# Optimization experiments

Hardware: AMD Instinct MI355X
Metric: run time of the kernel (lower is better)

Reference implementation:

```python
import jax, jax.numpy as jnp
import numpy as np

N_GRAM = 3
N_HEAD = 8


def setup_inputs() -> dict:
    key = jax.random.key(0)
    ks = jax.random.split(key, 8)
    V, E, H, H2, C, B, L = 50000, 512, 512, 512, 10, 64, 512
    def rn(k, shape, scale):
        return jax.random.normal(k, shape, jnp.float32) * jnp.float32(scale)
    return {
        "x": jax.random.randint(ks[0], (B, L), 0, V),
        "emb": rn(ks[1], (V, E), 0.02),
        "Wq": rn(ks[2], (H, E), 1.0 / np.sqrt(H)),
        "Wx": rn(ks[3], (E, 3 * H), 1.0 / np.sqrt(E)),
        "Wh": rn(ks[4], (H, 3 * H), 1.0 / np.sqrt(H)),
        "bx": jnp.zeros((3 * H,), jnp.float32),
        "bh": jnp.zeros((3 * H,), jnp.float32),
        "W1": rn(ks[5], (H, H2), 1.0 / np.sqrt(H)),
        "b1": jnp.zeros((H2,), jnp.float32),
        "W2": rn(ks[6], (H2, C), 1.0 / np.sqrt(H2)),
        "b2": jnp.zeros((C,), jnp.float32),
    }


def _gru_ngram_attn(xe, Wq, Wx, Wh, bx, bh):
    # xe: [B, L, E] embedded sequence
    B, L, E = xe.shape
    g, nh = N_GRAM, N_HEAD
    hd = E // nh
    H = Wh.shape[0]
    scale = jnp.float32(1.0 / np.sqrt(hd))
    xpad = jnp.pad(xe, ((0, 0), (g - 1, 0), (0, 0)))
    win = jnp.stack([xpad[:, i:i + L] for i in range(g)], axis=2)  # [B,L,g,E]
    win_t = jnp.transpose(win, (1, 0, 2, 3))  # [L,B,g,E] for scan
    h0 = jnp.zeros((B, H), xe.dtype)

    def step(h, w):
        # multi-head dot attention: query from prev hidden, keys/values = n-gram window
        q = (h @ Wq).reshape(B, nh, hd)          # [B,nh,hd]
        k = w.reshape(B, g, nh, hd)              # [B,g,nh,hd]
        scores = jnp.einsum('bnd,bgnd->bng', q, k) * scale
        a = jax.nn.softmax(scores, axis=-1)      # over window positions
        ctx = jnp.einsum('bng,bgnd->bnd', a, k).reshape(B, E)
        # GRU cell with attended context as input
        gx = ctx @ Wx + bx
        gh = h @ Wh + bh
        xr, xz, xn = jnp.split(gx, 3, axis=-1)
        hr, hz, hn = jnp.split(gh, 3, axis=-1)
        r = jax.nn.sigmoid(xr + hr)
        z = jax.nn.sigmoid(xz + hz)
        n = jnp.tanh(xn + r * hn)
        hnew = (1.0 - z) * n + z * h
        return hnew, hnew

    _, hs = jax.lax.scan(step, h0, win_t)  # [L,B,H]
    return hs


def reference(x, emb, Wq, Wx, Wh, bx, bh, W1, b1, W2, b2):
    xe = emb[x]  # [B,L,E]
    hs = _gru_ngram_attn(xe, Wq, Wx, Wh, bx, bh)  # [L,B,H]
    pooled = jax.nn.relu(hs.sum(axis=0))          # sum over seq, then relu
    out = pooled @ W1 + b1                        # fc1 path (H != embed not needed; H is GRU out)
    out = out @ W2 + b2                           # [B,C]
    return out
```

## Files before the change

kernel.cpp:

```cpp
#include <hip/hip_runtime.h>
#include <hip/hip_fp16.h>

typedef __attribute__((ext_vector_type(2))) _Float16 half2v;
typedef __attribute__((ext_vector_type(2))) __fp16   fp16x2;

#define SEQ     512
#define THREADS 512

#define WQ_OFF   0
#define WX_OFF   32768
#define WH_OFF   131072
#define SYNC_OFF 3670016

__device__ inline unsigned int pack2f16(float a, float b) {
    fp16x2 p = __builtin_amdgcn_cvt_pkrtz(a, b);
    return __builtin_bit_cast(unsigned int, p);
}
__device__ inline float fdot2u(unsigned int a, unsigned int b, float acc) {
    return __builtin_amdgcn_fdot2(__builtin_bit_cast(half2v, a),
                                  __builtin_bit_cast(half2v, b), acc, false);
}
__device__ inline float dot4(uint4 h, uint4 w, float acc) {
    acc = fdot2u(h.x, w.x, acc); acc = fdot2u(h.y, w.y, acc);
    acc = fdot2u(h.z, w.z, acc); acc = fdot2u(h.w, w.w, acc);
    return acc;
}
__device__ inline float fsigmoid(float x) { return 1.f / (1.f + __expf(-x)); }
__device__ inline float ftanhf(float x) {
    float e = __expf(-2.f * fabsf(x));
    float t = (1.f - e) / (1.f + e);
    return copysignf(t, x);
}
__device__ inline void vmem_fence() { asm volatile("s_waitcnt vmcnt(0)" ::: "memory"); }
__device__ inline unsigned a_ld(unsigned* p) {
    return __hip_atomic_load(p, __ATOMIC_RELAXED, __HIP_MEMORY_SCOPE_AGENT);
}
__device__ inline void a_st(unsigned* p, unsigned v) {
    __hip_atomic_store(p, v, __ATOMIC_RELAXED, __HIP_MEMORY_SCOPE_AGENT);
}
__device__ inline float a_ldf(float* p) {
    return __hip_atomic_load(p, __ATOMIC_RELAXED, __HIP_MEMORY_SCOPE_AGENT);
}
__device__ inline void a_stf(float* p, float v) {
    __hip_atomic_store(p, v, __ATOMIC_RELAXED, __HIP_MEMORY_SCOPE_AGENT);
}

__global__ __launch_bounds__(256)
void pack_weights(const float* __restrict__ Wq,
                  const float* __restrict__ Wx,
                  const float* __restrict__ Wh,
                  uint4* __restrict__ ws) {
    int tid = blockIdx.x * blockDim.x + threadIdx.x;
    const float* src; uint4* dst; int C, idx;
    if (tid < 64 * 512)                  { src = Wq; dst = ws;          C = 512;  idx = tid; }
    else if (tid < 64 * 512 + 64 * 1536) { src = Wx; dst = ws + WX_OFF; C = 1536; idx = tid - 64 * 512; }
    else                                 { src = Wh; dst = ws + WH_OFF; C = 1536; idx = tid - (64 * 512 + 64 * 1536); }
    int m4 = idx / C;
    int c  = idx - m4 * C;
    const float* s = src + (size_t)(m4 * 8) * C + c;
    uint4 o;
    o.x = pack2f16(s[0 * (size_t)C], s[1 * (size_t)C]);
    o.y = pack2f16(s[2 * (size_t)C], s[3 * (size_t)C]);
    o.z = pack2f16(s[4 * (size_t)C], s[5 * (size_t)C]);
    o.w = pack2f16(s[6 * (size_t)C], s[7 * (size_t)C]);
    dst[idx] = o;
}

__global__ __launch_bounds__(THREADS)
void gru_scan(const int* __restrict__ xtok, const float* __restrict__ emb,
              const uint4* __restrict__ wsp, const float* __restrict__ bx,
              const float* __restrict__ bh, const float* __restrict__ W1,
              const float* __restrict__ b1, const float* __restrict__ W2,
              const float* __restrict__ b2, float* __restrict__ out)
{
    const int blk  = blockIdx.x;
    const int gid  = blk & 7;
    const int bid  = blk >> 3;
    const int tid  = threadIdx.x;
    const int lane = tid & 63;
    const int wid  = tid >> 6;
    const int colsub = lane & 7;
    const int bp     = (lane >> 3) & 3;
    const int chsub  = lane >> 5;

    char* syncb = (char*)wsp + SYNC_OFF;
    unsigned* flagH = (unsigned*)syncb;
    unsigned* flagS = (unsigned*)(syncb + 1024);
    unsigned* Hbuf  = (unsigned*)(syncb + 2048);
    float* Pbuf     = (float*)(syncb + 133120);
    float* pooled_g = (float*)(syncb + 182272);
    float* fc1_g    = (float*)(syncb + 313344);

    __shared__ uint4 lds_W [64][65];
    __shared__ uint4 lds_Wx[64][49];
    __shared__ uint4 lds_h4[8][65];
    __shared__ unsigned u_pk[3][8][48][4];
    __shared__ float redQf[1152];
    __shared__ float redH[8][48][9];
    __shared__ float a_all[8][8][3];

    for (int i = tid; i < 64 * 64; i += THREADS) {
        int ch = i >> 6, cl = i & 63;
        uint4 v;
        if (cl < 16) v = wsp[WQ_OFF + ch * 512 + bid * 16 + cl];
        else { int g = (cl - 16) >> 4, c = (cl - 16) & 15;
               v = wsp[WH_OFF + ch * 1536 + g * 512 + bid * 16 + c]; }
        lds_W[ch][cl] = v;
    }
    for (int i = tid; i < 64 * 48; i += THREADS) {
        int ch = i / 48, cl = i - ch * 48;
        int g = cl >> 4, c = cl & 15;
        lds_Wx[ch][cl] = wsp[WX_OFF + ch * 1536 + g * 512 + bid * 16 + c];
    }

    float bxr = 0, bxz = 0, bxn = 0, bhr = 0, bhz = 0, bhn = 0;
    if (tid < 128) {
        int c = tid >> 3, cg = bid * 16 + c;
        bxr = bx[cg]; bxz = bx[512 + cg]; bxn = bx[1024 + cg];
        bhr = bh[cg]; bhz = bh[512 + cg]; bhn = bh[1024 + cg];
    }

    const int gb = gid * 8 + wid;
    {
        int tk = xtok[gb * SEQ];
        const float4* p = (const float4*)(emb + (size_t)tk * 512 + lane * 8);
        float4 ra = p[0], rb = p[1];
        uint4 pk;
        pk.x = pack2f16(ra.x, ra.y); pk.y = pack2f16(ra.z, ra.w);
        pk.z = pack2f16(rb.x, rb.y); pk.w = pack2f16(rb.z, rb.w);
        lds_h4[wid][lane] = pk;
        unsigned* up = &u_pk[0][0][0][0];
        for (int i = tid; i < 3072; i += THREADS) up[1536 + i] = 0u;
    }
    float hprev = 0.f, pooledv = 0.f;
    __syncthreads();

    for (int t = 0; t < SEQ; ++t) {
        const int par = t & 1;
        const int slot = t % 3;

        int tnext = (t + 1 < SEQ) ? (t + 1) : t;
        int tkn = xtok[gb * SEQ + tnext];
        const float4* pn = (const float4*)(emb + (size_t)tkn * 512 + lane * 8);
        float4 r3a = pn[0], r3b = pn[1];

        float winv[16];
        int b3 = 0, g3 = 0, trow = -1;
        if (wid == 0 && lane < 24) {
            b3 = lane / 3; g3 = lane - b3 * 3;
            trow = t - 2 + g3;
            int tok = (trow >= 0) ? xtok[(gid * 8 + b3) * SEQ + trow] : -1;
            if (tok >= 0) {
                const float* er = emb + (size_t)tok * 512 + bid * 16;
                #pragma unroll
                for (int d = 0; d < 16; ++d) winv[d] = er[d];
            } else {
                #pragma unroll
                for (int d = 0; d < 16; ++d) winv[d] = 0.f;
            }
        }

        {
            float acu[12];
            #pragma unroll
            for (int i = 0; i < 12; ++i) acu[i] = 0.f;
            int ch0 = wid * 8 + chsub * 4;
            #pragma unroll
            for (int i = 0; i < 4; ++i) {
                int ch = ch0 + i;
                uint4 c0 = lds_h4[bp][ch], c1 = lds_h4[bp + 4][ch];
                #pragma unroll
                for (int j = 0; j < 6; ++j) {
                    uint4 w = lds_Wx[ch][colsub + 8 * j];
                    acu[j]     = dot4(c0, w, acu[j]);
                    acu[6 + j] = dot4(c1, w, acu[6 + j]);
                }
            }
            #pragma unroll
            for (int i = 0; i < 12; ++i) acu[i] += __shfl_xor(acu[i], 32);
            if (chsub == 0) {
                #pragma unroll
                for (int j = 0; j < 6; ++j)
                    u_pk[slot][wid][colsub + 8 * j][bp] = pack2f16(acu[j], acu[6 + j]);
            }
        }

        if (wid == 0) {
            bool done = lane >= 32;
            while (!__all(done)) {
                if (!done) done = (a_ld(&flagH[gid * 32 + lane]) >= (unsigned)t);
                if (!__all(done)) __builtin_amdgcn_s_sleep(1);
            }
        }
        __syncthreads();

        {
            int bb = tid >> 6, c4 = tid & 63;
            unsigned* s = Hbuf + (size_t)(par ^ 1) * 16384 + (gid * 8 + bb) * 256 + c4 * 4;
            uint4 v;
            v.x = a_ld(s); v.y = a_ld(s + 1); v.z = a_ld(s + 2); v.w = a_ld(s + 3);
            lds_h4[bb][c4] = v;
        }
        __syncthreads();

        {
            float aq0 = 0, aq1 = 0, aq2 = 0, aq3 = 0;
            int ch0 = wid * 8 + chsub * 4;
            #pragma unroll
            for (int i = 0; i < 4; ++i) {
                int ch = ch0 + i;
                uint4 h0 = lds_h4[bp][ch], h1 = lds_h4[bp + 4][ch];
                uint4 w0 = lds_W[ch][colsub], w1 = lds_W[ch][colsub + 8];
                aq0 = dot4(h0, w0, aq0); aq1 = dot4(h0, w1, aq1);
                aq2 = dot4(h1, w0, aq2); aq3 = dot4(h1, w1, aq3);
            }
            aq0 += __shfl_xor(aq0, 32); aq1 += __shfl_xor(aq1, 32);
            aq2 += __shfl_xor(aq2, 32); aq3 += __shfl_xor(aq3, 32);
            if (chsub == 0) {
                redQf[(wid * 16 + colsub) * 9 + bp]         = aq0;
                redQf[(wid * 16 + colsub + 8) * 9 + bp]     = aq1;
                redQf[(wid * 16 + colsub) * 9 + bp + 4]     = aq2;
                redQf[(wid * 16 + colsub + 8) * 9 + bp + 4] = aq3;
            }
        }
        __syncthreads();

        if (wid == 0) {
            if (lane < 24) {
                float s = 0.f;
                if (trow >= 0) {
                    #pragma unroll
                    for (int d = 0; d < 16; ++d) {
                        float q = redQf[d * 9 + b3];
                        #pragma unroll
                        for (int k = 1; k < 8; ++k) q += redQf[(k * 16 + d) * 9 + b3];
                        s += winv[d] * q;
                    }
                }
                a_stf(&Pbuf[(size_t)((par * 8 + gid) * 32 + bid) * 24 + b3 * 3 + g3], s);
            }
            vmem_fence();
            if (lane == 0) a_st(&flagS[gid * 32 + bid], (unsigned)(t + 1));
            bool done = lane >= 32;
            while (!__all(done)) {
                if (!done) done = (a_ld(&flagS[gid * 32 + lane]) >= (unsigned)(t + 1));
                if (!__all(done)) __builtin_amdgcn_s_sleep(1);
            }
            {
                int bb = lane >> 3, n = lane & 7;
                float* pb = Pbuf + (size_t)(par * 8 + gid) * 32 * 24;
                float sc0 = 0, sc1 = 0, sc2 = 0;
                #pragma unroll
                for (int j = 0; j < 4; ++j) {
                    float* pj = pb + (n * 4 + j) * 24 + bb * 3;
                    sc0 += a_ldf(pj); sc1 += a_ldf(pj + 1); sc2 += a_ldf(pj + 2);
                }
                sc0 *= 0.125f; sc1 *= 0.125f; sc2 *= 0.125f;
                float mx = fmaxf(sc0, fmaxf(sc1, sc2));
                float e0 = __expf(sc0 - mx), e1 = __expf(sc1 - mx), e2 = __expf(sc2 - mx);
                float inv = 1.f / (e0 + e1 + e2);
                a_all[bb][n][0] = e0 * inv; a_all[bb][n][1] = e1 * inv; a_all[bb][n][2] = e2 * inv;
            }
        } else {
            #pragma unroll 1
            for (int rep = 0; rep < 2; ++rep) {
                int k = (rep == 0) ? wid : 0;
                if (rep == 1 && wid != 7) break;
                float ag[12];
                #pragma unroll
                for (int i = 0; i < 12; ++i) ag[i] = 0.f;
                int ch0 = k * 8 + chsub * 4;
                #pragma unroll
                for (int i = 0; i < 4; ++i) {
                    int ch = ch0 + i;
                    uint4 h0 = lds_h4[bp][ch], h1 = lds_h4[bp + 4][ch];
                    #pragma unroll
                    for (int j = 0; j < 6; ++j) {
                        uint4 w = lds_W[ch][16 + colsub + 8 * j];
                        ag[j]     = dot4(h0, w, ag[j]);
                        ag[6 + j] = dot4(h1, w, ag[6 + j]);
                    }
                }
                #pragma unroll
                for (int i = 0; i < 12; ++i) ag[i] += __shfl_xor(ag[i], 32);
                if (chsub == 0) {
                    #pragma unroll
                    for (int j = 0; j < 6; ++j) {
                        redH[k][colsub + 8 * j][bp]     = ag[j];
                        redH[k][colsub + 8 * j][bp + 4] = ag[6 + j];
                    }
                }
            }
        }
        __syncthreads();

        if (tid >= 64 && tid < 448) {
            int idx = tid - 64;
            int col = idx >> 3, bb = idx & 7;
            float ghs = redH[0][col][bb];
            #pragma unroll
            for (int k = 1; k < 8; ++k) ghs += redH[k][col][bb];
            float gxs = 0.f;
            int half = bb >> 2, bq = bb & 3;
            #pragma unroll
            for (int g = 0; g < 3; ++g) {
                int sg = (t + 1 + g) % 3;
                #pragma unroll
                for (int k = 0; k < 8; ++k) {
                    fp16x2 uv = __builtin_bit_cast(fp16x2, u_pk[sg][k][col][bq]);
                    gxs += a_all[bb][k][g] * (float)uv[half];
                }
            }
            redQf[col * 8 + bb]       = ghs;
            redQf[384 + col * 8 + bb] = gxs;
        }
        {
            uint4 pk;
            pk.x = pack2f16(r3a.x, r3a.y); pk.y = pack2f16(r3a.z, r3a.w);
            pk.z = pack2f16(r3b.x, r3b.y); pk.w = pack2f16(r3b.z, r3b.w);
            lds_h4[wid][lane] = pk;
        }
        __syncthreads();

        if (tid < 128) {
            int c = tid >> 3, bb = tid & 7;
            float ghr = redQf[c * 8 + bb]        + bhr;
            float ghz = redQf[(16 + c) * 8 + bb] + bhz;
            float ghn = redQf[(32 + c) * 8 + bb] + bhn;
            float gxr = redQf[384 + c * 8 + bb]        + bxr;
            float gxz = redQf[384 + (16 + c) * 8 + bb] + bxz;
            float gxn = redQf[384 + (32 + c) * 8 + bb] + bxn;
            float r = fsigmoid(gxr + ghr);
            float z = fsigmoid(gxz + ghz);
            float n = ftanhf(gxn + r * ghn);
            float hnew = (1.f - z) * n + z * hprev;
            hprev = hnew; pooledv += hnew;
            float hnext = __shfl_down(hnew, 8);
            if ((c & 1) == 0)
                a_st(&Hbuf[(size_t)par * 16384 + (gid * 8 + bb) * 256 + bid * 8 + (c >> 1)],
                     pack2f16(hnew, hnext));
        }
        vmem_fence();
        __syncthreads();
        if (tid == 0) a_st(&flagH[gid * 32 + bid], (unsigned)(t + 1));
    }

    float* stage = (float*)&lds_W[0][0];
    if (tid < 128) {
        int c = tid >> 3, bb = tid & 7;
        a_stf(&pooled_g[(gid * 8 + bb) * 512 + bid * 16 + c], fmaxf(pooledv, 0.f));
    }
    vmem_fence();
    __syncthreads();
    if (tid == 0) a_st(&flagS[gid * 32 + bid], (unsigned)(SEQ + 1));
    if (wid == 0) {
        bool done = lane >= 32;
        while (!__all(done)) {
            if (!done) done = (a_ld(&flagS[gid * 32 + lane]) >= (unsigned)(SEQ + 1));
            if (!__all(done)) __builtin_amdgcn_s_sleep(1);
        }
    }
    __syncthreads();

    for (int i = tid; i < 8 * 512; i += THREADS) {
        int bb = i >> 9, k = i & 511;
        stage[bb * 512 + k] = a_ldf(&pooled_g[(gid * 8 + bb) * 512 + k]);
    }
    __syncthreads();

    if (tid < 128) {
        int c = tid >> 3, bb = tid & 7;
        int cg = bid * 16 + c;
        const float* pr = stage + bb * 512;
        float acc1 = b1[cg];
        for (int k = 0; k < 512; ++k) acc1 += pr[k] * W1[(size_t)k * 512 + cg];
        a_stf(&fc1_g[(gid * 8 + bb) * 512 + cg], acc1);
    }
    vmem_fence();
    __syncthreads();
    if (tid == 0) a_st(&flagH[gid * 32 + bid], (unsigned)(SEQ + 2));

    if (bid == 0) {
        if (wid == 0) {
            bool done = lane >= 32;
            while (!__all(done)) {
                if (!done) done = (a_ld(&flagH[gid * 32 + lane]) >= (unsigned)(SEQ + 2));
                if (!__all(done)) __builtin_amdgcn_s_sleep(1);
            }
        }
        __syncthreads();
        for (int i = tid; i < 8 * 512; i += THREADS) {
            int bb = i >> 9, k = i & 511;
            stage[bb * 512 + k] = a_ldf(&fc1_g[(gid * 8 + bb) * 512 + k]);
        }
        __syncthreads();
        if (tid < 80) {
            int bb = tid / 10, cls = tid - bb * 10;
            const float* fr = stage + bb * 512;
            float a2 = b2[cls];
            for (int k = 0; k < 512; ++k) a2 += fr[k] * W2[k * 10 + cls];
            out[(gid * 8 + bb) * 10 + cls] = a2;
        }
    }
}

extern "C" void kernel_launch(void* const* d_in, const int* in_sizes, int n_in,
                              void* d_out, int out_size, void* d_ws, size_t ws_size,
                              hipStream_t stream) {
    const int*   x   = (const int*)d_in[0];
    const float* emb = (const float*)d_in[1];
    const float* Wq  = (const float*)d_in[2];
    const float* Wx  = (const float*)d_in[3];
    const float* Wh  = (const float*)d_in[4];
    const float* bx  = (const float*)d_in[5];
    const float* bh  = (const float*)d_in[6];
    const float* W1  = (const float*)d_in[7];
    const float* b1  = (const float*)d_in[8];
    const float* W2  = (const float*)d_in[9];
    const float* b2  = (const float*)d_in[10];
    uint4* wsp = (uint4*)d_ws;
    float* outp = (float*)d_out;

    hipLaunchKernelGGL(pack_weights, dim3(896), dim3(256), 0, stream, Wq, Wx, Wh, wsp);
    hipMemsetAsync((char*)d_ws + SYNC_OFF, 0, 182272, stream);

    void* args[] = { (void*)&x, (void*)&emb, (void*)&wsp, (void*)&bx, (void*)&bh,
                     (void*)&W1, (void*)&b1, (void*)&W2, (void*)&b2, (void*)&outp };
    hipError_t e = hipLaunchCooperativeKernel((void*)gru_scan, dim3(256), dim3(THREADS),
                                              args, 0, stream);
    if (e != hipSuccess) {
        hipLaunchKernelGGL(gru_scan, dim3(256), dim3(THREADS), 0, stream,
                           x, emb, wsp, bx, bh, W1, b1, W2, b2, outp);
    }
}
```

Baseline: 3.621 ms.

## Split each XCD's batch into two interleaved half-groups to overlap cross-block sync

```diff
diff --git a/kernel.cpp b/kernel.cpp
--- a/kernel.cpp
+++ b/kernel.cpp
@@ -74,30 +74,36 @@
               const float* __restrict__ b2, float* __restrict__ out)
 {
     const int blk  = blockIdx.x;
-    const int gid  = blk & 7;
+    const int xcd  = blk & 7;
     const int bid  = blk >> 3;
+    const int gA   = xcd * 2;
+    const int gB   = xcd * 2 + 1;
     const int tid  = threadIdx.x;
     const int lane = tid & 63;
-    const int wid  = tid >> 6;
+    const int w    = tid >> 6;
     const int colsub = lane & 7;
     const int bp     = (lane >> 3) & 3;
     const int chsub  = lane >> 5;
 
     char* syncb = (char*)wsp + SYNC_OFF;
     unsigned* flagH = (unsigned*)syncb;
-    unsigned* flagS = (unsigned*)(syncb + 1024);
-    unsigned* Hbuf  = (unsigned*)(syncb + 2048);
-    float* Pbuf     = (float*)(syncb + 133120);
-    float* pooled_g = (float*)(syncb + 182272);
-    float* fc1_g    = (float*)(syncb + 313344);
-
-    __shared__ uint4 lds_W [64][65];
-    __shared__ uint4 lds_Wx[64][49];
-    __shared__ uint4 lds_h4[8][65];
-    __shared__ unsigned u_pk[3][8][48][4];
-    __shared__ float redQf[1152];
-    __shared__ float redH[8][48][9];
-    __shared__ float a_all[8][8][3];
+    unsigned* flagS = (unsigned*)(syncb + 2048);
+    unsigned* Hbuf  = (unsigned*)(syncb + 4096);
+    float* Pbuf     = (float*)(syncb + 135168);
+    float* pooled_g = (float*)(syncb + 184320);
+    float* fc1_g    = (float*)(syncb + 315392);
+    unsigned* flagP = (unsigned*)(syncb + 446464);
+    unsigned* flagF = (unsigned*)(syncb + 447488);
+
+    __shared__ uint4 lds_W  [64][64];
+    __shared__ uint4 lds_Wx [64][48];
+    __shared__ uint4 lds_win[2][4][65];
+    __shared__ uint4 lds_hb [4][65];
+    __shared__ unsigned u_pk  [2][3][8][48][2];
+    __shared__ unsigned redH_pk[2][8][48][2];
+    __shared__ float redQf[640];
+    __shared__ float ghs[240], gxs[240];
+    __shared__ float a_all[2][4][8][3];
 
     for (int i = tid; i < 64 * 64; i += THREADS) {
         int ch = i >> 6, cl = i & 63;
@@ -115,283 +121,440 @@
 
     float bxr = 0, bxz = 0, bxn = 0, bhr = 0, bhz = 0, bhn = 0;
     if (tid < 128) {
-        int c = tid >> 3, cg = bid * 16 + c;
+        int m = (tid & 63) >> 2, cg = bid * 16 + m;
         bxr = bx[cg]; bxz = bx[512 + cg]; bxn = bx[1024 + cg];
         bhr = bh[cg]; bhz = bh[512 + cg]; bhn = bh[1024 + cg];
     }
 
-    const int gb = gid * 8 + wid;
+    const int wg  = w >> 2;
+    const int wb  = w & 3;
+    const int gbw = (xcd * 2 + wg) * 4 + wb;
+
     {
-        int tk = xtok[gb * SEQ];
+        int tk = xtok[gbw * SEQ];
         const float4* p = (const float4*)(emb + (size_t)tk * 512 + lane * 8);
         float4 ra = p[0], rb = p[1];
         uint4 pk;
         pk.x = pack2f16(ra.x, ra.y); pk.y = pack2f16(ra.z, ra.w);
         pk.z = pack2f16(rb.x, rb.y); pk.w = pack2f16(rb.z, rb.w);
-        lds_h4[wid][lane] = pk;
-        unsigned* up = &u_pk[0][0][0][0];
-        for (int i = tid; i < 3072; i += THREADS) up[1536 + i] = 0u;
+        lds_win[wg][wb][lane] = pk;
+        unsigned* up = &u_pk[0][0][0][0][0];
+        for (int i = tid; i < 2 * 1536; i += THREADS) {
+            int G = i / 1536, off = i - G * 1536;
+            up[G * 2304 + 768 + off] = 0u;
+        }
     }
     float hprev = 0.f, pooledv = 0.f;
     __syncthreads();
 
     for (int t = 0; t < SEQ; ++t) {
-        const int par = t & 1;
+        const int par  = t & 1;
         const int slot = t % 3;
 
-        int tnext = (t + 1 < SEQ) ? (t + 1) : t;
-        int tkn = xtok[gb * SEQ + tnext];
+        int tnext = (t + 1 < SEQ) ? t + 1 : t;
+        int tkn = xtok[gbw * SEQ + tnext];
         const float4* pn = (const float4*)(emb + (size_t)tkn * 512 + lane * 8);
         float4 r3a = pn[0], r3b = pn[1];
 
         float winv[16];
-        int b3 = 0, g3 = 0, trow = -1;
-        if (wid == 0 && lane < 24) {
-            b3 = lane / 3; g3 = lane - b3 * 3;
-            trow = t - 2 + g3;
-            int tok = (trow >= 0) ? xtok[(gid * 8 + b3) * SEQ + trow] : -1;
-            if (tok >= 0) {
-                const float* er = emb + (size_t)tok * 512 + bid * 16;
-                #pragma unroll
-                for (int d = 0; d < 16; ++d) winv[d] = er[d];
-            } else {
-                #pragma unroll
-                for (int d = 0; d < 16; ++d) winv[d] = 0.f;
-            }
-        }
-
-        {
-            float acu[12];
-            #pragma unroll
-            for (int i = 0; i < 12; ++i) acu[i] = 0.f;
-            int ch0 = wid * 8 + chsub * 4;
-            #pragma unroll
-            for (int i = 0; i < 4; ++i) {
-                int ch = ch0 + i;
-                uint4 c0 = lds_h4[bp][ch], c1 = lds_h4[bp + 4][ch];
-                #pragma unroll
-                for (int j = 0; j < 6; ++j) {
-                    uint4 w = lds_Wx[ch][colsub + 8 * j];
-                    acu[j]     = dot4(c0, w, acu[j]);
-                    acu[6 + j] = dot4(c1, w, acu[6 + j]);
-                }
-            }
-            #pragma unroll
-            for (int i = 0; i < 12; ++i) acu[i] += __shfl_xor(acu[i], 32);
-            if (chsub == 0) {
-                #pragma unroll
-                for (int j = 0; j < 6; ++j)
-                    u_pk[slot][wid][colsub + 8 * j][bp] = pack2f16(acu[j], acu[6 + j]);
-            }
-        }
-
-        if (wid == 0) {
+        int b3 = 0, g3 = 0, trow = -1, sgrp = -1;
+        if (w == 0) {
+            int l = -1;
+            if (lane < 12)                     { sgrp = 0; l = lane; }
+            else if (lane >= 32 && lane < 44)  { sgrp = 1; l = lane - 32; }
+            if (sgrp >= 0) {
+                b3 = l / 3; g3 = l - b3 * 3; trow = t - 2 + g3;
+                int gg = xcd * 2 + sgrp;
+                int tok = (trow >= 0) ? xtok[(gg * 4 + b3) * SEQ + trow] : -1;
+                if (tok >= 0) {
+                    const float* er = emb + (size_t)tok * 512 + bid * 16;
+                    #pragma unroll
+                    for (int d = 0; d < 16; ++d) winv[d] = er[d];
+                } else {
+                    #pragma unroll
+                    for (int d = 0; d < 16; ++d) winv[d] = 0.f;
+                }
+            }
+        }
+
+        uint4 hregA, hregB;
+
+        if (w == 0) {
             bool done = lane >= 32;
             while (!__all(done)) {
-                if (!done) done = (a_ld(&flagH[gid * 32 + lane]) >= (unsigned)t);
+                if (!done) done = (a_ld(&flagH[gA * 32 + lane]) >= (unsigned)t);
                 if (!__all(done)) __builtin_amdgcn_s_sleep(1);
-            }
-        }
-        __syncthreads();
-
-        {
-            int bb = tid >> 6, c4 = tid & 63;
-            unsigned* s = Hbuf + (size_t)(par ^ 1) * 16384 + (gid * 8 + bb) * 256 + c4 * 4;
-            uint4 v;
-            v.x = a_ld(s); v.y = a_ld(s + 1); v.z = a_ld(s + 2); v.w = a_ld(s + 3);
-            lds_h4[bb][c4] = v;
-        }
-        __syncthreads();
-
-        {
-            float aq0 = 0, aq1 = 0, aq2 = 0, aq3 = 0;
-            int ch0 = wid * 8 + chsub * 4;
-            #pragma unroll
-            for (int i = 0; i < 4; ++i) {
-                int ch = ch0 + i;
-                uint4 h0 = lds_h4[bp][ch], h1 = lds_h4[bp + 4][ch];
-                uint4 w0 = lds_W[ch][colsub], w1 = lds_W[ch][colsub + 8];
-                aq0 = dot4(h0, w0, aq0); aq1 = dot4(h0, w1, aq1);
-                aq2 = dot4(h1, w0, aq2); aq3 = dot4(h1, w1, aq3);
-            }
-            aq0 += __shfl_xor(aq0, 32); aq1 += __shfl_xor(aq1, 32);
-            aq2 += __shfl_xor(aq2, 32); aq3 += __shfl_xor(aq3, 32);
-            if (chsub == 0) {
-                redQf[(wid * 16 + colsub) * 9 + bp]         = aq0;
-                redQf[(wid * 16 + colsub + 8) * 9 + bp]     = aq1;
-                redQf[(wid * 16 + colsub) * 9 + bp + 4]     = aq2;
-                redQf[(wid * 16 + colsub + 8) * 9 + bp + 4] = aq3;
-            }
-        }
-        __syncthreads();
-
-        if (wid == 0) {
-            if (lane < 24) {
-                float s = 0.f;
-                if (trow >= 0) {
-                    #pragma unroll
-                    for (int d = 0; d < 16; ++d) {
-                        float q = redQf[d * 9 + b3];
-                        #pragma unroll
-                        for (int k = 1; k < 8; ++k) q += redQf[(k * 16 + d) * 9 + b3];
-                        s += winv[d] * q;
-                    }
-                }
-                a_stf(&Pbuf[(size_t)((par * 8 + gid) * 32 + bid) * 24 + b3 * 3 + g3], s);
-            }
-            vmem_fence();
-            if (lane == 0) a_st(&flagS[gid * 32 + bid], (unsigned)(t + 1));
-            bool done = lane >= 32;
-            while (!__all(done)) {
-                if (!done) done = (a_ld(&flagS[gid * 32 + lane]) >= (unsigned)(t + 1));
-                if (!__all(done)) __builtin_amdgcn_s_sleep(1);
-            }
-            {
-                int bb = lane >> 3, n = lane & 7;
-                float* pb = Pbuf + (size_t)(par * 8 + gid) * 32 * 24;
-                float sc0 = 0, sc1 = 0, sc2 = 0;
-                #pragma unroll
-                for (int j = 0; j < 4; ++j) {
-                    float* pj = pb + (n * 4 + j) * 24 + bb * 3;
-                    sc0 += a_ldf(pj); sc1 += a_ldf(pj + 1); sc2 += a_ldf(pj + 2);
-                }
-                sc0 *= 0.125f; sc1 *= 0.125f; sc2 *= 0.125f;
-                float mx = fmaxf(sc0, fmaxf(sc1, sc2));
-                float e0 = __expf(sc0 - mx), e1 = __expf(sc1 - mx), e2 = __expf(sc2 - mx);
-                float inv = 1.f / (e0 + e1 + e2);
-                a_all[bb][n][0] = e0 * inv; a_all[bb][n][1] = e1 * inv; a_all[bb][n][2] = e2 * inv;
             }
         } else {
             #pragma unroll 1
             for (int rep = 0; rep < 2; ++rep) {
-                int k = (rep == 0) ? wid : 0;
-                if (rep == 1 && wid != 7) break;
-                float ag[12];
-                #pragma unroll
-                for (int i = 0; i < 12; ++i) ag[i] = 0.f;
+                int k = (rep == 0) ? w : 0;
+                if (rep == 1 && w != 7) break;
+                float acu[6];
+                #pragma unroll
+                for (int i = 0; i < 6; ++i) acu[i] = 0.f;
                 int ch0 = k * 8 + chsub * 4;
                 #pragma unroll
                 for (int i = 0; i < 4; ++i) {
-                    int ch = ch0 + i;
-                    uint4 h0 = lds_h4[bp][ch], h1 = lds_h4[bp + 4][ch];
-                    #pragma unroll
-                    for (int j = 0; j < 6; ++j) {
-                        uint4 w = lds_W[ch][16 + colsub + 8 * j];
-                        ag[j]     = dot4(h0, w, ag[j]);
-                        ag[6 + j] = dot4(h1, w, ag[6 + j]);
+                    uint4 c0 = lds_win[0][bp][ch0 + i];
+                    #pragma unroll
+                    for (int j = 0; j < 6; ++j)
+                        acu[j] = dot4(c0, lds_Wx[ch0 + i][colsub + 8 * j], acu[j]);
+                }
+                #pragma unroll
+                for (int j = 0; j < 6; ++j) {
+                    acu[j] += __shfl_xor(acu[j], 32);
+                    float hi = __shfl_down(acu[j], 16);
+                    if (chsub == 0 && bp < 2)
+                        u_pk[0][slot][k][colsub + 8 * j][bp] = pack2f16(acu[j], hi);
+                }
+            }
+        }
+        __syncthreads();
+        if (tid < 256) {
+            int bb = tid >> 6, ch = tid & 63;
+            unsigned* s = Hbuf + (size_t)(par ^ 1) * 16384 + (gA * 4 + bb) * 256 + ch * 4;
+            hregA.x = a_ld(s); hregA.y = a_ld(s + 1); hregA.z = a_ld(s + 2); hregA.w = a_ld(s + 3);
+        }
+
+        if (w == 0) {
+            bool done = lane >= 32;
+            while (!__all(done)) {
+                if (!done) done = (a_ld(&flagH[gB * 32 + lane]) >= (unsigned)t);
+                if (!__all(done)) __builtin_amdgcn_s_sleep(1);
+            }
+        } else {
+            #pragma unroll 1
+            for (int rep = 0; rep < 2; ++rep) {
+                int k = (rep == 0) ? w : 0;
+                if (rep == 1 && w != 7) break;
+                float acu[6];
+                #pragma unroll
+                for (int i = 0; i < 6; ++i) acu[i] = 0.f;
+                int ch0 = k * 8 + chsub * 4;
+                #pragma unroll
+                for (int i = 0; i < 4; ++i) {
+                    uint4 c0 = lds_win[1][bp][ch0 + i];
+                    #pragma unroll
+                    for (int j = 0; j < 6; ++j)
+                        acu[j] = dot4(c0, lds_Wx[ch0 + i][colsub + 8 * j], acu[j]);
+                }
+                #pragma unroll
+                for (int j = 0; j < 6; ++j) {
+                    acu[j] += __shfl_xor(acu[j], 32);
+                    float hi = __shfl_down(acu[j], 16);
+                    if (chsub == 0 && bp < 2)
+                        u_pk[1][slot][k][colsub + 8 * j][bp] = pack2f16(acu[j], hi);
+                }
+            }
+        }
+        __syncthreads();
+        if (tid < 256) {
+            int bb = tid >> 6, ch = tid & 63;
+            unsigned* s = Hbuf + (size_t)(par ^ 1) * 16384 + (gB * 4 + bb) * 256 + ch * 4;
+            hregB.x = a_ld(s); hregB.y = a_ld(s + 1); hregB.z = a_ld(s + 2); hregB.w = a_ld(s + 3);
+        }
+
+        if (tid < 256) lds_hb[tid >> 6][tid & 63] = hregA;
+        __syncthreads();
+        {
+            float aq0 = 0, aq1 = 0;
+            int ch0 = w * 8 + chsub * 4;
+            #pragma unroll
+            for (int i = 0; i < 4; ++i) {
+                uint4 h0 = lds_hb[bp][ch0 + i];
+                aq0 = dot4(h0, lds_W[ch0 + i][colsub],     aq0);
+                aq1 = dot4(h0, lds_W[ch0 + i][colsub + 8], aq1);
+            }
+            aq0 += __shfl_xor(aq0, 32); aq1 += __shfl_xor(aq1, 32);
+            if (chsub == 0) {
+                redQf[w * 80 + colsub * 5 + bp]       = aq0;
+                redQf[w * 80 + (colsub + 8) * 5 + bp] = aq1;
+            }
+        }
+        __syncthreads();
+        if (w == 0) {
+            if (sgrp == 0) {
+                float s = 0.f;
+                if (trow >= 0) {
+                    #pragma unroll
+                    for (int d = 0; d < 16; ++d) {
+                        float q = redQf[d * 5 + b3];
+                        #pragma unroll
+                        for (int k = 1; k < 8; ++k) q += redQf[k * 80 + d * 5 + b3];
+                        s += winv[d] * q;
                     }
                 }
-                #pragma unroll
-                for (int i = 0; i < 12; ++i) ag[i] += __shfl_xor(ag[i], 32);
-                if (chsub == 0) {
-                    #pragma unroll
-                    for (int j = 0; j < 6; ++j) {
-                        redH[k][colsub + 8 * j][bp]     = ag[j];
-                        redH[k][colsub + 8 * j][bp + 4] = ag[6 + j];
+                a_stf(&Pbuf[((size_t)(par * 16 + gA) * 32 + bid) * 12 + b3 * 3 + g3], s);
+            }
+            vmem_fence();
+            if (lane == 0) a_st(&flagS[gA * 32 + bid], (unsigned)(t + 1));
+        } else {
+            #pragma unroll 1
+            for (int rep = 0; rep < 2; ++rep) {
+                int k = (rep == 0) ? w : 0;
+                if (rep == 1 && w != 7) break;
+                float ag[6];
+                #pragma unroll
+                for (int i = 0; i < 6; ++i) ag[i] = 0.f;
+                int ch0 = k * 8 + chsub * 4;
+                #pragma unroll
+                for (int i = 0; i < 4; ++i) {
+                    uint4 h0 = lds_hb[bp][ch0 + i];
+                    #pragma unroll
+                    for (int j = 0; j < 6; ++j)
+                        ag[j] = dot4(h0, lds_W[ch0 + i][16 + colsub + 8 * j], ag[j]);
+                }
+                #pragma unroll
+                for (int j = 0; j < 6; ++j) {
+                    ag[j] += __shfl_xor(ag[j], 32);
+                    float hi = __shfl_down(ag[j], 16);
+                    if (chsub == 0 && bp < 2)
+                        redH_pk[0][k][colsub + 8 * j][bp] = pack2f16(ag[j], hi);
+                }
+            }
+        }
+
+        __syncthreads();
+        if (tid < 256) lds_hb[tid >> 6][tid & 63] = hregB;
+        __syncthreads();
+        {
+            float aq0 = 0, aq1 = 0;
+            int ch0 = w * 8 + chsub * 4;
+            #pragma unroll
+            for (int i = 0; i < 4; ++i) {
+                uint4 h0 = lds_hb[bp][ch0 + i];
+                aq0 = dot4(h0, lds_W[ch0 + i][colsub],     aq0);
+                aq1 = dot4(h0, lds_W[ch0 + i][colsub + 8], aq1);
+            }
+            aq0 += __shfl_xor(aq0, 32); aq1 += __shfl_xor(aq1, 32);
+            if (chsub == 0) {
+                redQf[w * 80 + colsub * 5 + bp]       = aq0;
+                redQf[w * 80 + (colsub + 8) * 5 + bp] = aq1;
+            }
+        }
+        __syncthreads();
+        if (w == 0) {
+            if (sgrp == 1) {
+                float s = 0.f;
+                if (trow >= 0) {
+                    #pragma unroll
+                    for (int d = 0; d < 16; ++d) {
+                        float q = redQf[d * 5 + b3];
+                        #pragma unroll
+                        for (int k = 1; k < 8; ++k) q += redQf[k * 80 + d * 5 + b3];
+                        s += winv[d] * q;
                     }
                 }
-            }
-        }
-        __syncthreads();
-
-        if (tid >= 64 && tid < 448) {
-            int idx = tid - 64;
-            int col = idx >> 3, bb = idx & 7;
-            float ghs = redH[0][col][bb];
-            #pragma unroll
-            for (int k = 1; k < 8; ++k) ghs += redH[k][col][bb];
-            float gxs = 0.f;
-            int half = bb >> 2, bq = bb & 3;
-            #pragma unroll
-            for (int g = 0; g < 3; ++g) {
-                int sg = (t + 1 + g) % 3;
-                #pragma unroll
-                for (int k = 0; k < 8; ++k) {
-                    fp16x2 uv = __builtin_bit_cast(fp16x2, u_pk[sg][k][col][bq]);
-                    gxs += a_all[bb][k][g] * (float)uv[half];
-                }
-            }
-            redQf[col * 8 + bb]       = ghs;
-            redQf[384 + col * 8 + bb] = gxs;
+                a_stf(&Pbuf[((size_t)(par * 16 + gB) * 32 + bid) * 12 + b3 * 3 + g3], s);
+            }
+            vmem_fence();
+            if (lane == 0) a_st(&flagS[gB * 32 + bid], (unsigned)(t + 1));
+        } else {
+            #pragma unroll 1
+            for (int rep = 0; rep < 2; ++rep) {
+                int k = (rep == 0) ? w : 0;
+                if (rep == 1 && w != 7) break;
+                float ag[6];
+                #pragma unroll
+                for (int i = 0; i < 6; ++i) ag[i] = 0.f;
+                int ch0 = k * 8 + chsub * 4;
+                #pragma unroll
+                for (int i = 0; i < 4; ++i) {
+                    uint4 h0 = lds_hb[bp][ch0 + i];
+                    #pragma unroll
+                    for (int j = 0; j < 6; ++j)
+                        ag[j] = dot4(h0, lds_W[ch0 + i][16 + colsub + 8 * j], ag[j]);
+                }
+                #pragma unroll
+                for (int j = 0; j < 6; ++j) {
+                    ag[j] += __shfl_xor(ag[j], 32);
+                    float hi = __shfl_down(ag[j], 16);
+                    if (chsub == 0 && bp < 2)
+                        redH_pk[1][k][colsub + 8 * j][bp] = pack2f16(ag[j], hi);
+                }
+            }
+        }
+
+        if (w == 0) {
+            bool done = lane >= 32;
+            while (!__all(done)) {
+                if (!done) done = (a_ld(&flagS[gA * 32 + lane]) >= (unsigned)(t + 1));
+                if (!__all(done)) __builtin_amdgcn_s_sleep(1);
+            }
+            if (lane < 32) {
+                int b = lane >> 3, n = lane & 7;
+                float* base = Pbuf + (size_t)(par * 16 + gA) * 32 * 12;
+                float s0 = 0, s1 = 0, s2 = 0;
+                #pragma unroll
+                for (int j = 0; j < 4; ++j) {
+                    float* pj = base + (n * 4 + j) * 12 + b * 3;
+                    s0 += a_ldf(pj); s1 += a_ldf(pj + 1); s2 += a_ldf(pj + 2);
+                }
+                s0 *= 0.125f; s1 *= 0.125f; s2 *= 0.125f;
+                float mx = fmaxf(s0, fmaxf(s1, s2));
+                float e0 = __expf(s0 - mx), e1 = __expf(s1 - mx), e2 = __expf(s2 - mx);
+                float inv = 1.f / (e0 + e1 + e2);
+                a_all[0][b][n][0] = e0 * inv; a_all[0][b][n][1] = e1 * inv; a_all[0][b][n][2] = e2 * inv;
+            }
         }
         {
             uint4 pk;
             pk.x = pack2f16(r3a.x, r3a.y); pk.y = pack2f16(r3a.z, r3a.w);
             pk.z = pack2f16(r3b.x, r3b.y); pk.w = pack2f16(r3b.z, r3b.w);
-            lds_h4[wid][lane] = pk;
-        }
-        __syncthreads();
-
-        if (tid < 128) {
-            int c = tid >> 3, bb = tid & 7;
-            float ghr = redQf[c * 8 + bb]        + bhr;
-            float ghz = redQf[(16 + c) * 8 + bb] + bhz;
-            float ghn = redQf[(32 + c) * 8 + bb] + bhn;
-            float gxr = redQf[384 + c * 8 + bb]        + bxr;
-            float gxz = redQf[384 + (16 + c) * 8 + bb] + bxz;
-            float gxn = redQf[384 + (32 + c) * 8 + bb] + bxn;
-            float r = fsigmoid(gxr + ghr);
-            float z = fsigmoid(gxz + ghz);
-            float n = ftanhf(gxn + r * ghn);
+            lds_win[wg][wb][lane] = pk;
+        }
+        __syncthreads();
+        if (tid < 192) {
+            int col = tid >> 2, b = tid & 3;
+            int bq = b & 1, hf = b >> 1;
+            float ghsum = 0.f;
+            #pragma unroll
+            for (int k = 0; k < 8; ++k) {
+                fp16x2 v = __builtin_bit_cast(fp16x2, redH_pk[0][k][col][bq]);
+                ghsum += (float)v[hf];
+            }
+            float gxsum = 0.f;
+            #pragma unroll
+            for (int g = 0; g < 3; ++g) {
+                int sg = (t + 1 + g) % 3;
+                #pragma unroll
+                for (int k = 0; k < 8; ++k) {
+                    fp16x2 u = __builtin_bit_cast(fp16x2, u_pk[0][sg][k][col][bq]);
+                    gxsum += a_all[0][b][k][g] * (float)u[hf];
+                }
+            }
+            ghs[col * 5 + b] = ghsum;
+            gxs[col * 5 + b] = gxsum;
+        }
+        __syncthreads();
+        if (tid < 64) {
+            int m = tid >> 2, b = tid & 3;
+            float r = fsigmoid(gxs[m * 5 + b] + bxr + ghs[m * 5 + b] + bhr);
+            float z = fsigmoid(gxs[(16 + m) * 5 + b] + bxz + ghs[(16 + m) * 5 + b] + bhz);
+            float n = ftanhf(gxs[(32 + m) * 5 + b] + bxn + r * (ghs[(32 + m) * 5 + b] + bhn));
             float hnew = (1.f - z) * n + z * hprev;
             hprev = hnew; pooledv += hnew;
-            float hnext = __shfl_down(hnew, 8);
-            if ((c & 1) == 0)
-                a_st(&Hbuf[(size_t)par * 16384 + (gid * 8 + bb) * 256 + bid * 8 + (c >> 1)],
-                     pack2f16(hnew, hnext));
+            float hnx = __shfl_down(hnew, 4);
+            if (!(m & 1))
+                a_st(&Hbuf[(size_t)par * 16384 + (gA * 4 + b) * 256 + bid * 8 + (m >> 1)],
+                     pack2f16(hnew, hnx));
         }
         vmem_fence();
         __syncthreads();
-        if (tid == 0) a_st(&flagH[gid * 32 + bid], (unsigned)(t + 1));
-    }
-
-    float* stage = (float*)&lds_W[0][0];
+        if (tid == 0) a_st(&flagH[gA * 32 + bid], (unsigned)(t + 1));
+
+        if (w == 0) {
+            bool done = lane >= 32;
+            while (!__all(done)) {
+                if (!done) done = (a_ld(&flagS[gB * 32 + lane]) >= (unsigned)(t + 1));
+                if (!__all(done)) __builtin_amdgcn_s_sleep(1);
+            }
+            if (lane < 32) {
+                int b = lane >> 3, n = lane & 7;
+                float* base = Pbuf + (size_t)(par * 16 + gB) * 32 * 12;
+                float s0 = 0, s1 = 0, s2 = 0;
+                #pragma unroll
+                for (int j = 0; j < 4; ++j) {
+                    float* pj = base + (n * 4 + j) * 12 + b * 3;
+                    s0 += a_ldf(pj); s1 += a_ldf(pj + 1); s2 += a_ldf(pj + 2);
+                }
+                s0 *= 0.125f; s1 *= 0.125f; s2 *= 0.125f;
+                float mx = fmaxf(s0, fmaxf(s1, s2));
+                float e0 = __expf(s0 - mx), e1 = __expf(s1 - mx), e2 = __expf(s2 - mx);
+                float inv = 1.f / (e0 + e1 + e2);
+                a_all[1][b][n][0] = e0 * inv; a_all[1][b][n][1] = e1 * inv; a_all[1][b][n][2] = e2 * inv;
+            }
+        }
+        __syncthreads();
+        if (tid < 192) {
+            int col = tid >> 2, b = tid & 3;
+            int bq = b & 1, hf = b >> 1;
+            float ghsum = 0.f;
+            #pragma unroll
+            for (int k = 0; k < 8; ++k) {
+                fp16x2 v = __builtin_bit_cast(fp16x2, redH_pk[1][k][col][bq]);
+                ghsum += (float)v[hf];
+            }
+            float gxsum = 0.f;
+            #pragma unroll
+            for (int g = 0; g < 3; ++g) {
+                int sg = (t + 1 + g) % 3;
+                #pragma unroll
+                for (int k = 0; k < 8; ++k) {
+                    fp16x2 u = __builtin_bit_cast(fp16x2, u_pk[1][sg][k][col][bq]);
+                    gxsum += a_all[1][b][k][g] * (float)u[hf];
+                }
+            }
+            ghs[col * 5 + b] = ghsum;
+            gxs[col * 5 + b] = gxsum;
+        }
+        __syncthreads();
+        if (tid >= 64 && tid < 128) {
+            int m = (tid & 63) >> 2, b = (tid & 63) & 3;
+            float r = fsigmoid(gxs[m * 5 + b] + bxr + ghs[m * 5 + b] + bhr);
+            float z = fsigmoid(gxs[(16 + m) * 5 + b] + bxz + ghs[(16 + m) * 5 + b] + bhz);
+            float n = ftanhf(gxs[(32 + m) * 5 + b] + bxn + r * (ghs[(32 + m) * 5 + b] + bhn));
+            float hnew = (1.f - z) * n + z * hprev;
+            hprev = hnew; pooledv += hnew;
+            float hnx = __shfl_down(hnew, 4);
+            if (!(m & 1))
+                a_st(&Hbuf[(size_t)par * 16384 + (gB * 4 + b) * 256 + bid * 8 + (m >> 1)],
+                     pack2f16(hnew, hnx));
+        }
+        vmem_fence();
+        __syncthreads();
+        if (tid == 0) a_st(&flagH[gB * 32 + bid], (unsigned)(t + 1));
+    }
+
     if (tid < 128) {
-        int c = tid >> 3, bb = tid & 7;
-        a_stf(&pooled_g[(gid * 8 + bb) * 512 + bid * 16 + c], fmaxf(pooledv, 0.f));
+        int G = tid >> 6, l = tid & 63;
+        int m = l >> 2, b = l & 3;
+        int gb = (xcd * 2 + G) * 4 + b;
+        a_stf(&pooled_g[(size_t)gb * 512 + bid * 16 + m], fmaxf(pooledv, 0.f));
     }
     vmem_fence();
     __syncthreads();
-    if (tid == 0) a_st(&flagS[gid * 32 + bid], (unsigned)(SEQ + 1));
-    if (wid == 0) {
+    if (tid == 0) a_st(&flagP[blk], 1u);
+    if (w == 0) {
         bool done = lane >= 32;
         while (!__all(done)) {
-            if (!done) done = (a_ld(&flagS[gid * 32 + lane]) >= (unsigned)(SEQ + 1));
+            if (!done) done = (a_ld(&flagP[lane * 8 + xcd]) >= 1u);
             if (!__all(done)) __builtin_amdgcn_s_sleep(1);
         }
     }
     __syncthreads();
 
+    float* stage = (float*)&lds_W[0][0];
     for (int i = tid; i < 8 * 512; i += THREADS) {
         int bb = i >> 9, k = i & 511;
-        stage[bb * 512 + k] = a_ldf(&pooled_g[(gid * 8 + bb) * 512 + k]);
+        stage[i] = a_ldf(&pooled_g[(size_t)(xcd * 8 + bb) * 512 + k]);
     }
     __syncthreads();
-
     if (tid < 128) {
         int c = tid >> 3, bb = tid & 7;
         int cg = bid * 16 + c;
         const float* pr = stage + bb * 512;
         float acc1 = b1[cg];
         for (int k = 0; k < 512; ++k) acc1 += pr[k] * W1[(size_t)k * 512 + cg];
-        a_stf(&fc1_g[(gid * 8 + bb) * 512 + cg], acc1);
+        a_stf(&fc1_g[(size_t)(xcd * 8 + bb) * 512 + cg], acc1);
     }
     vmem_fence();
     __syncthreads();
-    if (tid == 0) a_st(&flagH[gid * 32 + bid], (unsigned)(SEQ + 2));
+    if (tid == 0) a_st(&flagF[blk], 1u);
 
     if (bid == 0) {
-        if (wid == 0) {
+        if (w == 0) {
             bool done = lane >= 32;
             while (!__all(done)) {
-                if (!done) done = (a_ld(&flagH[gid * 32 + lane]) >= (unsigned)(SEQ + 2));
+                if (!done) done = (a_ld(&flagF[lane * 8 + xcd]) >= 1u);
                 if (!__all(done)) __builtin_amdgcn_s_sleep(1);
             }
         }
         __syncthreads();
         for (int i = tid; i < 8 * 512; i += THREADS) {
             int bb = i >> 9, k = i & 511;
-            stage[bb * 512 + k] = a_ldf(&fc1_g[(gid * 8 + bb) * 512 + k]);
+            stage[i] = a_ldf(&fc1_g[(size_t)(xcd * 8 + bb) * 512 + k]);
         }
         __syncthreads();
         if (tid < 80) {
@@ -399,7 +562,7 @@
             const float* fr = stage + bb * 512;
             float a2 = b2[cls];
             for (int k = 0; k < 512; ++k) a2 += fr[k] * W2[k * 10 + cls];
-            out[(gid * 8 + bb) * 10 + cls] = a2;
+            out[(xcd * 8 + bb) * 10 + cls] = a2;
         }
     }
 }
@@ -422,7 +585,8 @@
     float* outp = (float*)d_out;
 
     hipLaunchKernelGGL(pack_weights, dim3(896), dim3(256), 0, stream, Wq, Wx, Wh, wsp);
-    hipMemsetAsync((char*)d_ws + SYNC_OFF, 0, 182272, stream);
+    hipMemsetAsync((char*)d_ws + SYNC_OFF, 0, 135168, stream);
+    hipMemsetAsync((char*)d_ws + SYNC_OFF + 446464, 0, 2048, stream);
 
     void* args[] = { (void*)&x, (void*)&emb, (void*)&wsp, (void*)&bx, (void*)&bh,
                      (void*)&W1, (void*)&b1, (void*)&W2, (void*)&b2, (void*)&outp };
```

Measured after the change: 6.248 ms. 1.73x slower.
